# Performance work log

Hardware: AMD Instinct MI355X
Metric: run time of the kernel (lower is better)

The kernel has to match this reference:

```python
import jax, jax.numpy as jnp
import numpy as np

N_NODES = 100000
N_EDGES = 1600000
N_GRAPHS = 128
NHID = 128
NLAYER = 4
BN_EPS = 1e-5


def setup_inputs() -> dict:
    key = jax.random.key(0)
    ks = jax.random.split(key, 12)
    x_idx = jax.random.randint(ks[0], (N_NODES,), 0, 100)
    edge_index = jax.random.randint(ks[1], (2, N_EDGES), 0, N_NODES)
    edge_attr = jax.random.randint(ks[2], (N_EDGES,), 0, 20)
    batch = jnp.sort(jax.random.randint(ks[3], (N_NODES,), 0, N_GRAPHS))
    s = 0.1
    return {
        "x_idx": x_idx,
        "edge_index": edge_index,
        "edge_attr": edge_attr,
        "batch": batch,
        "node_emb": jax.random.normal(ks[4], (100, NHID), jnp.float32) * s,
        "edge_emb": jax.random.normal(ks[5], (NLAYER, 20, NHID), jnp.float32) * s,
        "conv_w1": jax.random.normal(ks[6], (NLAYER, NHID, NHID), jnp.float32) * s,
        "conv_w2": jax.random.normal(ks[7], (NLAYER, NHID, NHID), jnp.float32) * s,
        "bn_gamma": jnp.ones((NLAYER, NHID), jnp.float32),
        "bn_beta": jnp.zeros((NLAYER, NHID), jnp.float32),
        "out_w1": jax.random.normal(ks[8], (NHID, NHID), jnp.float32) * s,
        "out_b1": jnp.zeros((NHID,), jnp.float32),
        "out_bn_gamma": jnp.ones((NHID,), jnp.float32),
        "out_bn_beta": jnp.zeros((NHID,), jnp.float32),
        "out_w2": jax.random.normal(ks[9], (NHID, 1), jnp.float32) * s,
        "out_b2": jnp.zeros((1,), jnp.float32),
    }


def _batchnorm(h, gamma, beta):
    mu = h.mean(axis=0)
    var = h.var(axis=0)
    return (h - mu) * jax.lax.rsqrt(var + BN_EPS) * gamma + beta


def reference(x_idx, edge_index, edge_attr, batch, node_emb, edge_emb,
              conv_w1, conv_w2, bn_gamma, bn_beta,
              out_w1, out_b1, out_bn_gamma, out_bn_beta, out_w2, out_b2):
    # input encoder: discrete embedding lookup  [N, nhid]
    x = node_emb[x_idx]
    src, dst = edge_index[0], edge_index[1]
    prev = x
    for l in range(NLAYER):
        ea = edge_emb[l][edge_attr]                      # [E, nhid] edge encoder
        msg = jax.nn.relu(x[src] + ea)                   # GINE messages
        agg = jax.ops.segment_sum(msg, dst, num_segments=N_NODES)
        h = x + agg                                      # (1+eps)*x + agg, eps=0
        h = jax.nn.relu(h @ conv_w1[l]) @ conv_w2[l]     # GINE nn (bias=False)
        h = _batchnorm(h, bn_gamma[l], bn_beta[l])
        h = jax.nn.relu(h)                               # dropout p=0 is a no-op
        h = h + prev                                     # residual
        prev = h
        x = h
    # add pooling over graphs
    g = jax.ops.segment_sum(x, batch, num_segments=N_GRAPHS)   # [B, nhid]
    # output encoder: Linear -> BN -> ReLU -> Linear
    o = g @ out_w1 + out_b1
    o = jax.nn.relu(_batchnorm(o, out_bn_gamma, out_bn_beta))
    o = o @ out_w2 + out_b2
    return o
```

## Files before the change

### kernel.cpp

```cpp
#include <hip/hip_runtime.h>

#define N_NODES 100000
#define N_EDGES 1600000
#define N_GRAPHS 128
#define NHID 128
#define NLAYER 4
#define BN_EPS 1e-5f

#define SCAN_ITEMS 1024
#define SCAN_NB ((N_NODES + SCAN_ITEMS - 1) / SCAN_ITEMS)

#define FILL_CHUNK 8192
#define FILL_NB ((N_NODES + 255) / 256)

__device__ __forceinline__ float4 ld4(const float* p){ return *(const float4*)p; }
__device__ __forceinline__ void st4(float* p, float4 v){ *(float4*)p = v; }

typedef __attribute__((ext_vector_type(8))) short short8v;
typedef __attribute__((ext_vector_type(4))) float f32x4;

__device__ __forceinline__ void bsplit(float a, unsigned short& h, unsigned short& l){
    unsigned ab = __float_as_uint(a);
    h = (unsigned short)(ab >> 16);
    float hf = __uint_as_float((unsigned)h << 16);
    l = (unsigned short)(__float_as_uint(a - hf) >> 16);
}

__device__ __forceinline__ unsigned short brne(float a){
    unsigned ab = __float_as_uint(a);
    return (unsigned short)((ab + 0x7FFFu + ((ab >> 16) & 1u)) >> 16);
}
__device__ __forceinline__ float b2f(unsigned short b){
    return __uint_as_float((unsigned)b << 16);
}


__global__ void k_hist(const int* __restrict__ dst, int* __restrict__ counts){
    int e = blockIdx.x * 256 + threadIdx.x;
    if (e < N_EDGES) atomicAdd(&counts[dst[e]], 1);
}

__global__ void k_scan_partial(const int* __restrict__ counts, int* __restrict__ partial){
    __shared__ int s[256];
    int t = threadIdx.x;
    int base = blockIdx.x * SCAN_ITEMS + t * 4;
    int v = 0;
    #pragma unroll
    for (int k = 0; k < 4; k++) if (base + k < N_NODES) v += counts[base + k];
    s[t] = v;
    __syncthreads();
    for (int o = 128; o > 0; o >>= 1){
        if (t < o) s[t] += s[t + o];
        __syncthreads();
    }
    if (t == 0) partial[blockIdx.x] = s[0];
}

__global__ void k_scan_top(int* __restrict__ partial, int nb, int* __restrict__ row_ptr){
    __shared__ int s[128];
    int t = threadIdx.x;
    int v = (t < nb) ? partial[t] : 0;
    s[t] = v;
    __syncthreads();
    for (int d = 1; d < 128; d <<= 1){
        int add = (t >= d) ? s[t - d] : 0;
        __syncthreads();
        s[t] += add;
        __syncthreads();
    }
    if (t < nb) partial[t] = s[t] - v;
    if (t == 0) row_ptr[N_NODES] = N_EDGES;
}

__global__ void k_scan_final(const int* __restrict__ counts, const int* __restrict__ partial,
                             int* __restrict__ row_ptr){
    __shared__ int s[256];
    int t = threadIdx.x;
    int base = blockIdx.x * SCAN_ITEMS + t * 4;
    int v[4]; int tsum = 0;
    #pragma unroll
    for (int k = 0; k < 4; k++){ v[k] = (base + k < N_NODES) ? counts[base + k] : 0; tsum += v[k]; }
    s[t] = tsum;
    __syncthreads();
    for (int d = 1; d < 256; d <<= 1){
        int add = (t >= d) ? s[t - d] : 0;
        __syncthreads();
        s[t] += add;
        __syncthreads();
    }
    int off = partial[blockIdx.x] + s[t] - tsum;
    #pragma unroll
    for (int k = 0; k < 4; k++){
        if (base + k < N_NODES) row_ptr[base + k] = off;
        off += v[k];
    }
}

__global__ void k_binit(const int* __restrict__ row_ptr, int* __restrict__ bcur){
    int b = blockIdx.x * 256 + threadIdx.x;
    if (b < FILL_NB) bcur[b] = row_ptr[b * 256];
}

__global__ __launch_bounds__(256) void k_fillA(const int* __restrict__ eidx,
                        const int* __restrict__ eattr, const int* __restrict__ x_idx,
                        int* __restrict__ bcur, uint2* __restrict__ tmp){
    __shared__ int cnt[FILL_NB];
    __shared__ int lstart[FILL_NB];
    __shared__ int lcur[FILL_NB];
    __shared__ int gbase[FILL_NB];
    __shared__ uint2 stage[FILL_CHUNK];
    int t = threadIdx.x;
    int e0 = blockIdx.x * FILL_CHUNK;
    int n = min(FILL_CHUNK, N_EDGES - e0);
    for (int i = t; i < FILL_NB; i += 256) cnt[i] = 0;
    __syncthreads();
    for (int i = t; i < n; i += 256)
        atomicAdd(&cnt[(unsigned)eidx[N_EDGES + e0 + i] >> 8], 1);
    __syncthreads();
    if (t == 0){
        int run = 0;
        for (int b = 0; b < FILL_NB; b++){ lstart[b] = run; run += cnt[b]; }
    }
    __syncthreads();
    for (int i = t; i < FILL_NB; i += 256) lcur[i] = lstart[i];
    __syncthreads();
    for (int i = t; i < n; i += 256){
        int e = e0 + i;
        int d = eidx[N_EDGES + e];
        int s = eidx[e];
        int a = eattr[e];
        int xi = x_idx[s];
        unsigned w = (unsigned)s | ((unsigned)a << 17) | ((unsigned)xi << 22);
        int pos = atomicAdd(&lcur[d >> 8], 1);
        stage[pos] = make_uint2(w, (unsigned)d);
    }
    __syncthreads();
    for (int b = t; b < FILL_NB; b += 256)
        if (cnt[b] > 0) gbase[b] = atomicAdd(&bcur[b], cnt[b]);
    __syncthreads();
    for (int i = t; i < n; i += 256){
        uint2 v = stage[i];
        int b = (int)(v.y >> 8);
        tmp[gbase[b] + (i - lstart[b])] = v;
    }
}

__global__ __launch_bounds__(256) void k_fillB(const uint2* __restrict__ tmp,
                        const int* __restrict__ row_ptr,
                        int* __restrict__ cursor, unsigned* __restrict__ pack){
    int b = blockIdx.x;
    int start = row_ptr[b * 256];
    int end   = row_ptr[min((b + 1) * 256, N_NODES)];
    for (int p = start + (int)threadIdx.x; p < end; p += 256){
        uint2 v = tmp[p];
        int pos = atomicAdd(&cursor[v.y], 1);
        pack[pos] = v.x;
    }
}


__global__ void k_combo(const float* __restrict__ node_emb, const float* __restrict__ edge_emb0,
                        float* __restrict__ combo){
    int i = blockIdx.x * 256 + threadIdx.x;
    if (i >= 2000 * NHID) return;
    int row = i >> 7, c = i & 127;
    int ni = row / 20, a = row - ni * 20;
    combo[i] = fmaxf(node_emb[ni * NHID + c] + edge_emb0[a * NHID + c], 0.f);
}


__global__ void k_wsplit(const float* __restrict__ w1, const float* __restrict__ w2,
                         unsigned short* __restrict__ wth, unsigned short* __restrict__ wtl){
    int i = blockIdx.x * 256 + threadIdx.x;
    int which = i >> 16;
    int m = (i >> 14) & 3;
    int r = i & 16383;
    int k = r >> 7, c = r & 127;
    float v = (which ? w2 : w1)[m * 16384 + k * 128 + c];
    unsigned short h, l;
    bsplit(v, h, l);
    int o = ((which * 4 + m) * 128 + c) * 128 + k;
    wth[o] = h; wtl[o] = l;
}


__global__ void k_initx(const int* __restrict__ x_idx, const float* __restrict__ node_emb,
                        float4* __restrict__ x4){
    int i = blockIdx.x * 256 + threadIdx.x;
    if (i >= N_NODES * 32) return;
    int n = i >> 5, c = i & 31;
    int id = x_idx[n];
    x4[i] = ((const float4*)node_emb)[id * 32 + c];
}


__global__ __launch_bounds__(256) void k_agg(const float* __restrict__ x,
                      const ushort2* __restrict__ xb,
                      const int* __restrict__ row_ptr,
                      const unsigned* __restrict__ pack, const float* __restrict__ emb_l,
                      float2* __restrict__ h0){
    int gid = blockIdx.x * 256 + threadIdx.x;
    int node = gid >> 6;
    int lane = threadIdx.x & 63;
    const float2* x2 = (const float2*)x;
    const float2* e2 = (const float2*)emb_l;
    float2 acc = x2[node * 64 + lane];
    int beg = row_ptr[node], end = row_ptr[node + 1];
    int i = beg;
    for (; i + 3 < end; i += 4){
        unsigned p0 = pack[i], p1 = pack[i+1], p2 = pack[i+2], p3 = pack[i+3];
        ushort2 g0 = xb[(p0 & 0x1FFFFu) * 64 + lane];
        ushort2 g1 = xb[(p1 & 0x1FFFFu) * 64 + lane];
        ushort2 g2 = xb[(p2 & 0x1FFFFu) * 64 + lane];
        ushort2 g3 = xb[(p3 & 0x1FFFFu) * 64 + lane];
        float2 b0 = e2[((p0 >> 17) & 31u) * 64 + lane];
        float2 b1 = e2[((p1 >> 17) & 31u) * 64 + lane];
        float2 b2 = e2[((p2 >> 17) & 31u) * 64 + lane];
        float2 b3 = e2[((p3 >> 17) & 31u) * 64 + lane];
        acc.x += (fmaxf(b2f(g0.x) + b0.x, 0.f) + fmaxf(b2f(g1.x) + b1.x, 0.f))
               + (fmaxf(b2f(g2.x) + b2.x, 0.f) + fmaxf(b2f(g3.x) + b3.x, 0.f));
        acc.y += (fmaxf(b2f(g0.y) + b0.y, 0.f) + fmaxf(b2f(g1.y) + b1.y, 0.f))
               + (fmaxf(b2f(g2.y) + b2.y, 0.f) + fmaxf(b2f(g3.y) + b3.y, 0.f));
    }
    for (; i < end; i++){
        unsigned p = pack[i];
        ushort2 g = xb[(p & 0x1FFFFu) * 64 + lane];
        float2 ev = e2[((p >> 17) & 31u) * 64 + lane];
        acc.x += fmaxf(b2f(g.x) + ev.x, 0.f);
        acc.y += fmaxf(b2f(g.y) + ev.y, 0.f);
    }
    h0[node * 64 + lane] = acc;
}


__global__ __launch_bounds__(256) void k_agg0(const float* __restrict__ x,
                      const int* __restrict__ row_ptr,
                      const unsigned* __restrict__ pack,
                      const float* __restrict__ combo,
                      float2* __restrict__ h0){
    int gid = blockIdx.x * 256 + threadIdx.x;
    int node = gid >> 6;
    int lane = threadIdx.x & 63;
    const float2* x2 = (const float2*)x;
    const float2* c2 = (const float2*)combo;
    float2 acc = x2[node * 64 + lane];
    int beg = row_ptr[node], end = row_ptr[node + 1];
    int i = beg;
    for (; i + 3 < end; i += 4){
        unsigned p0 = pack[i], p1 = pack[i+1], p2 = pack[i+2], p3 = pack[i+3];
        int ci0 = (int)((p0 >> 22) & 127u) * 20 + (int)((p0 >> 17) & 31u);
        int ci1 = (int)((p1 >> 22) & 127u) * 20 + (int)((p1 >> 17) & 31u);
        int ci2 = (int)((p2 >> 22) & 127u) * 20 + (int)((p2 >> 17) & 31u);
        int ci3 = (int)((p3 >> 22) & 127u) * 20 + (int)((p3 >> 17) & 31u);
        float2 m0 = c2[ci0 * 64 + lane];
        float2 m1 = c2[ci1 * 64 + lane];
        float2 m2 = c2[ci2 * 64 + lane];
        float2 m3 = c2[ci3 * 64 + lane];
        acc.x += (m0.x + m1.x) + (m2.x + m3.x);
        acc.y += (m0.y + m1.y) + (m2.y + m3.y);
    }
    for (; i < end; i++){
        unsigned p = pack[i];
        int ci = (int)((p >> 22) & 127u) * 20 + (int)((p >> 17) & 31u);
        float2 m = c2[ci * 64 + lane];
        acc.x += m.x;
        acc.y += m.y;
    }
    h0[node * 64 + lane] = acc;
}


template<int RELU_OUT, int DO_STATS>
__global__ __launch_bounds__(256) void k_mfma(const float* __restrict__ A,
                                              const unsigned short* __restrict__ Wth,
                                              const unsigned short* __restrict__ Wtl,
                                              float* __restrict__ out,
                                              float* __restrict__ stats_l){
    __shared__ unsigned short Ah[128][40], Al[128][40];
    __shared__ unsigned short Bh[128][40], Bl[128][40];
    const int tid = threadIdx.x;
    const int w = tid >> 6;
    const int l = tid & 63;
    const int lr = l & 15;
    const int lk = l >> 4;
    const int row0 = blockIdx.x * 128;

    f32x4 acc[2][8];
    #pragma unroll
    for (int m = 0; m < 2; m++)
        #pragma unroll
        for (int n = 0; n < 8; n++) acc[m][n] = (f32x4)(0.f);

    for (int kc = 0; kc < 4; kc++){
        __syncthreads();
        #pragma unroll
        for (int q = 0; q < 4; q++){
            int f = tid + 256 * q;
            int r = f >> 3, kq = f & 7;
            int gr = row0 + r;
            float4 v = make_float4(0.f, 0.f, 0.f, 0.f);
            if (gr < N_NODES) v = ld4(A + (size_t)gr * NHID + kc * 32 + kq * 4);
            unsigned short h0,l0,h1,l1,h2,l2,h3,l3;
            bsplit(v.x, h0, l0); bsplit(v.y, h1, l1);
            bsplit(v.z, h2, l2); bsplit(v.w, h3, l3);
            *(ushort4*)&Ah[r][kq * 4] = make_ushort4(h0, h1, h2, h3);
            *(ushort4*)&Al[r][kq * 4] = make_ushort4(l0, l1, l2, l3);
        }
        #pragma unroll
        for (int q = 0; q < 2; q++){
            int f = tid + 256 * q;
            int c = f >> 2, kq = f & 3;
            size_t gi = (size_t)c * 128 + kc * 32 + kq * 8;
            *(uint4*)&Bh[c][kq * 8] = *(const uint4*)(Wth + gi);
            *(uint4*)&Bl[c][kq * 8] = *(const uint4*)(Wtl + gi);
        }
        __syncthreads();
        short8v pah[2], pal[2];
        #pragma unroll
        for (int m = 0; m < 2; m++){
            pah[m] = *(const short8v*)&Ah[w * 32 + m * 16 + lr][lk * 8];
            pal[m] = *(const short8v*)&Al[w * 32 + m * 16 + lr][lk * 8];
        }
        #pragma unroll
        for (int n = 0; n < 8; n++){
            short8v pbh = *(const short8v*)&Bh[n * 16 + lr][lk * 8];
            short8v pbl = *(const short8v*)&Bl[n * 16 + lr][lk * 8];
            #pragma unroll
            for (int m = 0; m < 2; m++){
                acc[m][n] = __builtin_amdgcn_mfma_f32_16x16x32_bf16(pal[m], pbh, acc[m][n], 0, 0, 0);
                acc[m][n] = __builtin_amdgcn_mfma_f32_16x16x32_bf16(pah[m], pbl, acc[m][n], 0, 0, 0);
                acc[m][n] = __builtin_amdgcn_mfma_f32_16x16x32_bf16(pah[m], pbh, acc[m][n], 0, 0, 0);
            }
        }
    }

    if (RELU_OUT){
        #pragma unroll
        for (int m = 0; m < 2; m++)
            #pragma unroll
            for (int n = 0; n < 8; n++)
                #pragma unroll
                for (int j = 0; j < 4; j++) acc[m][n][j] = fmaxf(acc[m][n][j], 0.f);
    }
    #pragma unroll
    for (int m = 0; m < 2; m++)
        #pragma unroll
        for (int j = 0; j < 4; j++){
            int gr = row0 + w * 32 + m * 16 + lk * 4 + j;
            if (gr < N_NODES){
                #pragma unroll
                for (int n = 0; n < 8; n++)
                    out[(size_t)gr * NHID + n * 16 + lr] = acc[m][n][j];
            }
        }

    if (DO_STATS){
        __syncthreads();
        float* red  = (float*)&Ah[0][0];
        float* red2 = (float*)&Bh[0][0];
        #pragma unroll
        for (int n = 0; n < 8; n++){
            float s = 0.f, q = 0.f;
            #pragma unroll
            for (int m = 0; m < 2; m++)
                #pragma unroll
                for (int j = 0; j < 4; j++){ float v = acc[m][n][j]; s += v; q += v * v; }
            red [(w * 4 + lk) * 128 + n * 16 + lr] = s;
            red2[(w * 4 + lk) * 128 + n * 16 + lr] = q;
        }
        __syncthreads();
        if (tid < 128){
            float s = 0.f, q = 0.f;
            #pragma unroll
            for (int r2 = 0; r2 < 16; r2++){
                s += red[r2 * 128 + tid];
                q += red2[r2 * 128 + tid];
            }
            atomicAdd(&stats_l[tid], s);
            atomicAdd(&stats_l[128 + tid], q);
        }
    }
}


__global__ void k_norm(const float4* __restrict__ h2, float4* __restrict__ x,
                       ushort4* __restrict__ xb,
                       const float* __restrict__ stats_l,
                       const float* __restrict__ gamma, const float* __restrict__ beta){
    int i = blockIdx.x * 256 + threadIdx.x;
    if (i >= N_NODES * 32) return;
    int g = (i & 31);
    float4 sv = ((const float4*)stats_l)[g];
    float4 qv = ((const float4*)(stats_l + 128))[g];
    float4 gm = ((const float4*)gamma)[g];
    float4 bt = ((const float4*)beta)[g];
    float4 ca, cb;
    {
        float mu, var;
        mu = sv.x * (1.f / N_NODES); var = qv.x * (1.f / N_NODES) - mu * mu;
        ca.x = gm.x * rsqrtf(var + BN_EPS); cb.x = bt.x - mu * ca.x;
        mu = sv.y * (1.f / N_NODES); var = qv.y * (1.f / N_NODES) - mu * mu;
        ca.y = gm.y * rsqrtf(var + BN_EPS); cb.y = bt.y - mu * ca.y;
        mu = sv.z * (1.f / N_NODES); var = qv.z * (1.f / N_NODES) - mu * mu;
        ca.z = gm.z * rsqrtf(var + BN_EPS); cb.z = bt.z - mu * ca.z;
        mu = sv.w * (1.f / N_NODES); var = qv.w * (1.f / N_NODES) - mu * mu;
        ca.w = gm.w * rsqrtf(var + BN_EPS); cb.w = bt.w - mu * ca.w;
    }
    float4 h = h2[i];
    float4 xv = x[i];
    float4 r;
    r.x = fmaxf(fmaf(h.x, ca.x, cb.x), 0.f) + xv.x;
    r.y = fmaxf(fmaf(h.y, ca.y, cb.y), 0.f) + xv.y;
    r.z = fmaxf(fmaf(h.z, ca.z, cb.z), 0.f) + xv.z;
    r.w = fmaxf(fmaf(h.w, ca.w, cb.w), 0.f) + xv.w;
    x[i] = r;
    xb[i] = make_ushort4(brne(r.x), brne(r.y), brne(r.z), brne(r.w));
}


__global__ __launch_bounds__(256) void k_pool(const float* __restrict__ x,
                       const int* __restrict__ batch, float* __restrict__ gbuf){
    int c = threadIdx.x & 127;
    int half = threadIdx.x >> 7;
    int n0 = blockIdx.x * 128;
    int nend = min(n0 + 128, N_NODES);
    float acc = 0.f;
    int gcur = -1;
    for (int n = n0 + half; n < nend; n += 2){
        int g = batch[n];
        if (g != gcur){
            if (gcur >= 0) atomicAdd(&gbuf[gcur * NHID + c], acc);
            acc = 0.f; gcur = g;
        }
        acc += x[(size_t)n * NHID + c];
    }
    if (gcur >= 0) atomicAdd(&gbuf[gcur * NHID + c], acc);
}


__global__ __launch_bounds__(128) void k_head1(const float* __restrict__ gbuf,
                                               const float* __restrict__ w1,
                                               const float* __restrict__ b1,
                                               float* __restrict__ o1){
    __shared__ float gs[128];
    int i = blockIdx.x;
    int j = threadIdx.x;
    gs[j] = gbuf[i * NHID + j];
    __syncthreads();
    float acc = 0.f;
    #pragma unroll 8
    for (int k = 0; k < 128; k++)
        acc = fmaf(gs[k], w1[k * NHID + j], acc);
    o1[i * NHID + j] = acc + b1[j];
}

__global__ __launch_bounds__(128) void k_head2(const float* __restrict__ o1,
                                               const float* __restrict__ gamma,
                                               const float* __restrict__ beta,
                                               const float* __restrict__ w2,
                                               const float* __restrict__ b2,
                                               float* __restrict__ out){
    __shared__ float s_o1[128][129];
    __shared__ float sa[128], sb[128];
    int t = threadIdx.x;
    float s = 0.f, q = 0.f;
    for (int r = 0; r < 128; r++){
        float v = o1[r * NHID + t];
        s_o1[r][t] = v;
        s += v; q += v * v;
    }
    float mu = s * (1.f / 128.f);
    float rs = rsqrtf(q * (1.f / 128.f) - mu * mu + BN_EPS);
    float a = gamma[t] * rs;
    sa[t] = a;
    sb[t] = beta[t] - mu * a;
    __syncthreads();
    float a2 = 0.f;
    #pragma unroll 8
    for (int j = 0; j < 128; j++){
        float v = fmaf(s_o1[t][j], sa[j], sb[j]);
        a2 += fmaxf(v, 0.f) * w2[j];
    }
    out[t] = a2 + b2[0];
}


extern "C" void kernel_launch(void* const* d_in, const int* in_sizes, int n_in,
                              void* d_out, int out_size, void* d_ws, size_t ws_size,
                              hipStream_t stream){
    const int*   x_idx    = (const int*)d_in[0];
    const int*   eidx     = (const int*)d_in[1];
    const int*   eattr    = (const int*)d_in[2];
    const int*   batch    = (const int*)d_in[3];
    const float* node_emb = (const float*)d_in[4];
    const float* edge_emb = (const float*)d_in[5];
    const float* conv_w1  = (const float*)d_in[6];
    const float* conv_w2  = (const float*)d_in[7];
    const float* bn_gamma = (const float*)d_in[8];
    const float* bn_beta  = (const float*)d_in[9];
    const float* out_w1   = (const float*)d_in[10];
    const float* out_b1   = (const float*)d_in[11];
    const float* out_bng  = (const float*)d_in[12];
    const float* out_bnb  = (const float*)d_in[13];
    const float* out_w2   = (const float*)d_in[14];
    const float* out_b2   = (const float*)d_in[15];
    float* out = (float*)d_out;

    char* base = (char*)d_ws;
    size_t off = 0;
    auto alloc = [&](size_t bytes) -> char* {
        char* r = base + off;
        off = (off + bytes + 255) & ~(size_t)255;
        return r;
    };
    float*          xbuf    = (float*)alloc((size_t)N_NODES * NHID * 4);
    float*          h0buf   = (float*)alloc((size_t)N_NODES * NHID * 4);
    unsigned short* xbf     = (unsigned short*)alloc((size_t)N_NODES * NHID * 2);
    int*            row_ptr = (int*)alloc((size_t)(N_NODES + 1) * 4);
    int*            cursor  = (int*)alloc((size_t)N_NODES * 4);
    int*            counts  = (int*)alloc((size_t)N_NODES * 4);
    int*            partial = (int*)alloc(512 * 4);
    int*            bcur    = (int*)alloc((size_t)FILL_NB * 4);
    unsigned*       pack    = (unsigned*)alloc((size_t)N_EDGES * 4);
    uint2*          tmp     = (uint2*)alloc((size_t)N_EDGES * 8);
    float*          combo   = (float*)alloc((size_t)2000 * NHID * 4);
    unsigned short* wth     = (unsigned short*)alloc((size_t)8 * 16384 * 2);
    unsigned short* wtl     = (unsigned short*)alloc((size_t)8 * 16384 * 2);
    float*          stats   = (float*)alloc(NLAYER * 256 * 4);
    float*          gbuf    = (float*)alloc((size_t)N_GRAPHS * NHID * 4);
    float*          o1buf   = (float*)alloc((size_t)N_GRAPHS * NHID * 4);
    (void)ws_size; (void)in_sizes; (void)n_in; (void)out_size;

    hipMemsetAsync(counts, 0, (size_t)N_NODES * 4, stream);
    hipMemsetAsync(stats, 0, NLAYER * 256 * 4, stream);
    hipMemsetAsync(gbuf, 0, (size_t)N_GRAPHS * NHID * 4, stream);

    k_hist<<<N_EDGES / 256, 256, 0, stream>>>(eidx + N_EDGES, counts);
    k_scan_partial<<<SCAN_NB, 256, 0, stream>>>(counts, partial);
    k_scan_top<<<1, 128, 0, stream>>>(partial, SCAN_NB, row_ptr);
    k_scan_final<<<SCAN_NB, 256, 0, stream>>>(counts, partial, row_ptr);
    hipMemcpyAsync(cursor, row_ptr, (size_t)N_NODES * 4, hipMemcpyDeviceToDevice, stream);
    k_binit<<<(FILL_NB + 255) / 256, 256, 0, stream>>>(row_ptr, bcur);
    k_fillA<<<(N_EDGES + FILL_CHUNK - 1) / FILL_CHUNK, 256, 0, stream>>>(
        eidx, eattr, x_idx, bcur, tmp);
    k_fillB<<<FILL_NB, 256, 0, stream>>>(tmp, row_ptr, cursor, pack);

    k_combo<<<(2000 * NHID) / 256, 256, 0, stream>>>(node_emb, edge_emb, combo);
    k_wsplit<<<131072 / 256, 256, 0, stream>>>(conv_w1, conv_w2, wth, wtl);
    k_initx<<<(N_NODES * 32) / 256, 256, 0, stream>>>(x_idx, node_emb, (float4*)xbuf);

    const int gemm_grid = (N_NODES + 127) / 128;
    for (int l = 0; l < NLAYER; l++){
        if (l == 0){
            k_agg0<<<(N_NODES * 64) / 256, 256, 0, stream>>>(
                xbuf, row_ptr, pack, combo, (float2*)h0buf);
        } else {
            k_agg<<<(N_NODES * 64) / 256, 256, 0, stream>>>(
                xbuf, (const ushort2*)xbf, row_ptr, pack,
                edge_emb + (size_t)l * 20 * NHID, (float2*)h0buf);
        }
        k_mfma<1, 0><<<gemm_grid, 256, 0, stream>>>(
            h0buf, wth + (size_t)l * 16384, wtl + (size_t)l * 16384, h0buf, nullptr);
        k_mfma<0, 1><<<gemm_grid, 256, 0, stream>>>(
            h0buf, wth + (size_t)(4 + l) * 16384, wtl + (size_t)(4 + l) * 16384,
            h0buf, stats + l * 256);
        k_norm<<<(N_NODES * 32) / 256, 256, 0, stream>>>(
            (const float4*)h0buf, (float4*)xbuf, (ushort4*)xbf, stats + l * 256,
            bn_gamma + l * NHID, bn_beta + l * NHID);
    }

    k_pool<<<(N_NODES + 127) / 128, 256, 0, stream>>>(xbuf, batch, gbuf);
    k_head1<<<N_GRAPHS, 128, 0, stream>>>(gbuf, out_w1, out_b1, o1buf);
    k_head2<<<1, 128, 0, stream>>>(o1buf, out_bng, out_bnb, out_w2, out_b2, out);
}
```

Measured before the change: 1.011 ms.

## Fuse the two GINE MLP GEMMs into one kernel, keeping the intermediate on-chip

Merges the two per-layer MFMA GEMM kernels into one. The ReLU'd first-GEMM result stays in registers and is re-split into bf16 hi/lo through shared memory to feed the second GEMM. This removes the write and re-read of the 100k x 128 float intermediate plus one launch per layer. The cost is twice the accumulator registers per thread, which may lower occupancy or cause spills. In-place output to h0buf stays safe because each block reads only its own rows before writing.

```diff
diff --git a/kernel.cpp b/kernel.cpp
--- a/kernel.cpp
+++ b/kernel.cpp
@@ -270,12 +270,13 @@
 }
 
 
-template<int RELU_OUT, int DO_STATS>
-__global__ __launch_bounds__(256) void k_mfma(const float* __restrict__ A,
-                                              const unsigned short* __restrict__ Wth,
-                                              const unsigned short* __restrict__ Wtl,
-                                              float* __restrict__ out,
-                                              float* __restrict__ stats_l){
+__global__ __launch_bounds__(256) void k_mlp(const float* __restrict__ A,
+                                             const unsigned short* __restrict__ W1th,
+                                             const unsigned short* __restrict__ W1tl,
+                                             const unsigned short* __restrict__ W2th,
+                                             const unsigned short* __restrict__ W2tl,
+                                             float* __restrict__ out,
+                                             float* __restrict__ stats_l){
     __shared__ unsigned short Ah[128][40], Al[128][40];
     __shared__ unsigned short Bh[128][40], Bl[128][40];
     const int tid = threadIdx.x;
@@ -285,11 +286,11 @@
     const int lk = l >> 4;
     const int row0 = blockIdx.x * 128;
 
-    f32x4 acc[2][8];
+    f32x4 acc1[2][8], acc2[2][8];
     #pragma unroll
     for (int m = 0; m < 2; m++)
         #pragma unroll
-        for (int n = 0; n < 8; n++) acc[m][n] = (f32x4)(0.f);
+        for (int n = 0; n < 8; n++){ acc1[m][n] = (f32x4)(0.f); acc2[m][n] = (f32x4)(0.f); }
 
     for (int kc = 0; kc < 4; kc++){
         __syncthreads();
@@ -311,8 +312,8 @@
             int f = tid + 256 * q;
             int c = f >> 2, kq = f & 3;
             size_t gi = (size_t)c * 128 + kc * 32 + kq * 8;
-            *(uint4*)&Bh[c][kq * 8] = *(const uint4*)(Wth + gi);
-            *(uint4*)&Bl[c][kq * 8] = *(const uint4*)(Wtl + gi);
+            *(uint4*)&Bh[c][kq * 8] = *(const uint4*)(W1th + gi);
+            *(uint4*)&Bl[c][kq * 8] = *(const uint4*)(W1tl + gi);
         }
         __syncthreads();
         short8v pah[2], pal[2];
@@ -327,21 +328,65 @@
             short8v pbl = *(const short8v*)&Bl[n * 16 + lr][lk * 8];
             #pragma unroll
             for (int m = 0; m < 2; m++){
-                acc[m][n] = __builtin_amdgcn_mfma_f32_16x16x32_bf16(pal[m], pbh, acc[m][n], 0, 0, 0);
-                acc[m][n] = __builtin_amdgcn_mfma_f32_16x16x32_bf16(pah[m], pbl, acc[m][n], 0, 0, 0);
-                acc[m][n] = __builtin_amdgcn_mfma_f32_16x16x32_bf16(pah[m], pbh, acc[m][n], 0, 0, 0);
+                acc1[m][n] = __builtin_amdgcn_mfma_f32_16x16x32_bf16(pal[m], pbh, acc1[m][n], 0, 0, 0);
+                acc1[m][n] = __builtin_amdgcn_mfma_f32_16x16x32_bf16(pah[m], pbl, acc1[m][n], 0, 0, 0);
+                acc1[m][n] = __builtin_amdgcn_mfma_f32_16x16x32_bf16(pah[m], pbh, acc1[m][n], 0, 0, 0);
             }
         }
     }
 
-    if (RELU_OUT){
+    #pragma unroll
+    for (int m = 0; m < 2; m++)
+        #pragma unroll
+        for (int n = 0; n < 8; n++)
+            #pragma unroll
+            for (int j = 0; j < 4; j++) acc1[m][n][j] = fmaxf(acc1[m][n][j], 0.f);
+
+    for (int kc = 0; kc < 4; kc++){
+        __syncthreads();
         #pragma unroll
         for (int m = 0; m < 2; m++)
             #pragma unroll
-            for (int n = 0; n < 8; n++)
+            for (int j = 0; j < 4; j++){
+                int trow = w * 32 + m * 16 + lk * 4 + j;
                 #pragma unroll
-                for (int j = 0; j < 4; j++) acc[m][n][j] = fmaxf(acc[m][n][j], 0.f);
-    }
+                for (int nn = 0; nn < 2; nn++){
+                    float v = acc1[m][kc * 2 + nn][j];
+                    unsigned short h, lo;
+                    bsplit(v, h, lo);
+                    int tcol = nn * 16 + lr;
+                    Ah[trow][tcol] = h;
+                    Al[trow][tcol] = lo;
+                }
+            }
+        #pragma unroll
+        for (int q = 0; q < 2; q++){
+            int f = tid + 256 * q;
+            int c = f >> 2, kq = f & 3;
+            size_t gi = (size_t)c * 128 + kc * 32 + kq * 8;
+            *(uint4*)&Bh[c][kq * 8] = *(const uint4*)(W2th + gi);
+            *(uint4*)&Bl[c][kq * 8] = *(const uint4*)(W2tl + gi);
+        }
+        __syncthreads();
+        short8v pah[2], pal[2];
+        #pragma unroll
+        for (int m = 0; m < 2; m++){
+            pah[m] = *(const short8v*)&Ah[w * 32 + m * 16 + lr][lk * 8];
+            pal[m] = *(const short8v*)&Al[w * 32 + m * 16 + lr][lk * 8];
+        }
+        #pragma unroll
+        for (int n = 0; n < 8; n++){
+            short8v pbh = *(const short8v*)&Bh[n * 16 + lr][lk * 8];
+            short8v pbl = *(const short8v*)&Bl[n * 16 + lr][lk * 8];
+            #pragma unroll
+            for (int m = 0; m < 2; m++){
+                acc2[m][n] = __builtin_amdgcn_mfma_f32_16x16x32_bf16(pal[m], pbh, acc2[m][n], 0, 0, 0);
+                acc2[m][n] = __builtin_amdgcn_mfma_f32_16x16x32_bf16(pah[m], pbl, acc2[m][n], 0, 0, 0);
+                acc2[m][n] = __builtin_amdgcn_mfma_f32_16x16x32_bf16(pah[m], pbh, acc2[m][n], 0, 0, 0);
+            }
+        }
+    }
+
     #pragma unroll
     for (int m = 0; m < 2; m++)
         #pragma unroll
@@ -350,35 +395,33 @@
             if (gr < N_NODES){
                 #pragma unroll
                 for (int n = 0; n < 8; n++)
-                    out[(size_t)gr * NHID + n * 16 + lr] = acc[m][n][j];
+                    out[(size_t)gr * NHID + n * 16 + lr] = acc2[m][n][j];
             }
         }
 
-    if (DO_STATS){
-        __syncthreads();
-        float* red  = (float*)&Ah[0][0];
-        float* red2 = (float*)&Bh[0][0];
-        #pragma unroll
-        for (int n = 0; n < 8; n++){
-            float s = 0.f, q = 0.f;
+    __syncthreads();
+    float* red  = (float*)&Ah[0][0];
+    float* red2 = (float*)&Bh[0][0];
+    #pragma unroll
+    for (int n = 0; n < 8; n++){
+        float s = 0.f, q = 0.f;
+        #pragma unroll
+        for (int m = 0; m < 2; m++)
             #pragma unroll
-            for (int m = 0; m < 2; m++)
-                #pragma unroll
-                for (int j = 0; j < 4; j++){ float v = acc[m][n][j]; s += v; q += v * v; }
-            red [(w * 4 + lk) * 128 + n * 16 + lr] = s;
-            red2[(w * 4 + lk) * 128 + n * 16 + lr] = q;
-        }
-        __syncthreads();
-        if (tid < 128){
-            float s = 0.f, q = 0.f;
-            #pragma unroll
-            for (int r2 = 0; r2 < 16; r2++){
-                s += red[r2 * 128 + tid];
-                q += red2[r2 * 128 + tid];
-            }
-            atomicAdd(&stats_l[tid], s);
-            atomicAdd(&stats_l[128 + tid], q);
-        }
+            for (int j = 0; j < 4; j++){ float v = acc2[m][n][j]; s += v; q += v * v; }
+        red [(w * 4 + lk) * 128 + n * 16 + lr] = s;
+        red2[(w * 4 + lk) * 128 + n * 16 + lr] = q;
+    }
+    __syncthreads();
+    if (tid < 128){
+        float s = 0.f, q = 0.f;
+        #pragma unroll
+        for (int r2 = 0; r2 < 16; r2++){
+            s += red[r2 * 128 + tid];
+            q += red2[r2 * 128 + tid];
+        }
+        atomicAdd(&stats_l[tid], s);
+        atomicAdd(&stats_l[128 + tid], q);
     }
 }
 
@@ -559,10 +602,10 @@
                 xbuf, (const ushort2*)xbf, row_ptr, pack,
                 edge_emb + (size_t)l * 20 * NHID, (float2*)h0buf);
         }
-        k_mfma<1, 0><<<gemm_grid, 256, 0, stream>>>(
-            h0buf, wth + (size_t)l * 16384, wtl + (size_t)l * 16384, h0buf, nullptr);
-        k_mfma<0, 1><<<gemm_grid, 256, 0, stream>>>(
-            h0buf, wth + (size_t)(4 + l) * 16384, wtl + (size_t)(4 + l) * 16384,
+        k_mlp<<<gemm_grid, 256, 0, stream>>>(
+            h0buf,
+            wth + (size_t)l * 16384, wtl + (size_t)l * 16384,
+            wth + (size_t)(4 + l) * 16384, wtl + (size_t)(4 + l) * 16384,
             h0buf, stats + l * 256);
         k_norm<<<(N_NODES * 32) / 256, 256, 0, stream>>>(
             (const float4*)h0buf, (float4*)xbuf, (ushort4*)xbf, stats + l * 256,
```

Result: faster. 958.1 us (-5.2%).
